# Optimization experiments

Hardware: AMD Instinct MI355X
Metric: run time of the kernel (lower is better)

The kernel has to match this reference:

```python
import jax, jax.numpy as jnp
import numpy as np

DIM = 512
D_STATE = 16
D_CONV = 4
EXPAND = 2
D_INNER = EXPAND * DIM  # 1024
BATCH = 4
SEQLEN = 4096


def silu(v):
    return v * jax.nn.sigmoid(v)


def setup_inputs() -> dict:
    key = jax.random.key(0)
    ks = jax.random.split(key, 8)
    s = 0.02  # small init scale for stability
    return {
        "x": jax.random.normal(ks[0], (BATCH, SEQLEN, DIM), jnp.float32),
        "W_in": jax.random.normal(ks[1], (2 * D_INNER, DIM), jnp.float32) * s,
        "conv_w": jax.random.normal(ks[2], (D_INNER, 1, D_CONV), jnp.float32) * s,
        "conv_b": jax.random.normal(ks[3], (D_INNER,), jnp.float32) * s,
        "W_x": jax.random.normal(ks[4], (2 * D_STATE, D_INNER), jnp.float32) * s,
        "W_dt": jax.random.normal(ks[5], (D_STATE, D_INNER), jnp.float32) * s,
        "b_dt": jax.random.normal(ks[6], (D_STATE,), jnp.float32) * s,
        "A_log": jnp.log(jnp.arange(1, D_STATE + 1, dtype=jnp.float32))[None, :],
        "D_param": jnp.ones((D_INNER,), jnp.float32),
        "W_out": jax.random.normal(ks[7], (DIM, D_INNER), jnp.float32) * s,
    }


def reference(x, W_in, conv_w, conv_b, W_x, W_dt, b_dt, A_log, D_param, W_out):
    B, L, _ = x.shape
    # in_proj and split into x / res streams
    x_and_res = jnp.einsum('bld,ed->ble', x, W_in)          # [B,L,2*d_inner]
    xi, res = x_and_res[..., :D_INNER], x_and_res[..., D_INNER:]
    # causal depthwise conv1d (torch pads both sides by d_conv-1 then slices [:L]
    # == left-pad d_conv-1, no right pad)
    xc = jax.lax.conv_general_dilated(
        xi.transpose(0, 2, 1), conv_w, (1,), [(D_CONV - 1, 0)],
        dimension_numbers=('NCH', 'OIH', 'NCH'), feature_group_count=D_INNER)
    xa = silu(xc.transpose(0, 2, 1) + conv_b)               # [B,L,d_inner]
    # x_proj: first d_state (dt) half is discarded in the source; keep B half
    B_proj = jnp.einsum('bld,ed->ble', xa, W_x)[..., D_STATE:]  # [B,L,N]
    dt = jax.nn.softplus(jnp.einsum('bld,nd->bln', xa, W_dt) + b_dt)  # [B,L,N]
    A = -jnp.exp(A_log.reshape(-1))                         # [N]
    A_disc = jnp.exp(A * dt)                                # [B,L,N]
    d_rep = D_INNER // D_STATE
    u = jnp.mean(xa[..., :d_rep], axis=-1)                  # [B,L] scalar drive
    Bu = (dt * B_proj) * u[..., None]                       # [B,L,N]

    def step(s, ab):
        a, b = ab
        s = s * a + b
        return s, s

    s0 = jnp.zeros((B, D_STATE), xa.dtype)
    _, y = jax.lax.scan(step, s0, (A_disc.transpose(1, 0, 2), Bu.transpose(1, 0, 2)))
    y = y.transpose(1, 0, 2)                                # [B,L,N]
    y = jnp.repeat(y, d_rep, axis=-1)                       # [B,L,d_inner]
    y = y + xa * D_param
    y = y * silu(res)
    return jnp.einsum('bld,ed->ble', y, W_out)              # [B,L,dim]
```

## Files before the change

kernel.cpp:

```cpp
#include <hip/hip_runtime.h>
#include <stdint.h>

typedef __bf16 bf16_t;
typedef __bf16 bf16x8 __attribute__((ext_vector_type(8)));
typedef __bf16 bf16x4 __attribute__((ext_vector_type(4)));
typedef float  f32x4  __attribute__((ext_vector_type(4)));

#define AS1 __attribute__((address_space(1)))
#define AS3 __attribute__((address_space(3)))

#define SEQ   4096
#define DIMM  512
#define DIN   1024
#define ROWS  16384

__device__ __forceinline__ void gload_lds16(const void* g, void* l) {
  __builtin_amdgcn_global_load_lds((AS1 void*)g, (AS3 void*)l, 16, 0, 0);
}

template<bool OUT_BF16>
__global__ void gemm_bt(const bf16_t* __restrict__ A, const bf16_t* __restrict__ B,
                        void* __restrict__ Cv, int lda, int N, int K)
{
  __shared__ __align__(16) bf16_t As[128*64];
  __shared__ __align__(16) bf16_t Bs[128*64];
  const int tid = threadIdx.x;
  const int l = tid & 63, w = tid >> 6;
  const int bm = blockIdx.x, bn = blockIdx.y;
  const bf16_t* Ab = A + (size_t)bm*128*lda;
  const bf16_t* Bb = B + (size_t)bn*128*K;
  f32x4 acc[4][4] = {};
  const int wr = (w>>1)*64, wc = (w&1)*64;
  const int lr = l & 15, lk = (l>>4)*8;
  const int srow = w*8 + (l>>3);
  const int scol = (l&7)*8;

  for (int kt = 0; kt < K; kt += 64) {
#pragma unroll
    for (int i = 0; i < 4; i++) {
      gload_lds16(Ab + (size_t)(i*32 + srow)*lda + kt + scol, As + i*2048 + w*512);
      gload_lds16(Bb + (size_t)(i*32 + srow)*K   + kt + scol, Bs + i*2048 + w*512);
    }
    __syncthreads();
#pragma unroll
    for (int kk = 0; kk < 2; kk++) {
      bf16x8 af[4], bv[4];
#pragma unroll
      for (int m = 0; m < 4; m++) af[m] = *(const bf16x8*)&As[(wr + m*16 + lr)*64 + kk*32 + lk];
#pragma unroll
      for (int n = 0; n < 4; n++) bv[n] = *(const bf16x8*)&Bs[(wc + n*16 + lr)*64 + kk*32 + lk];
#pragma unroll
      for (int m = 0; m < 4; m++)
#pragma unroll
        for (int n = 0; n < 4; n++)
          acc[m][n] = __builtin_amdgcn_mfma_f32_16x16x32_bf16(af[m], bv[n], acc[m][n], 0, 0, 0);
    }
    __syncthreads();
  }
  const int row0 = bm*128 + wr + (l>>4)*4;
  const int col0 = bn*128 + wc + lr;
#pragma unroll
  for (int m = 0; m < 4; m++)
#pragma unroll
    for (int n = 0; n < 4; n++)
#pragma unroll
      for (int r = 0; r < 4; r++) {
        size_t idx = (size_t)(row0 + m*16 + r)*N + (col0 + n*16);
        if constexpr (OUT_BF16) ((bf16_t*)Cv)[idx] = (bf16_t)acc[m][n][r];
        else                    ((float*)Cv)[idx]  = acc[m][n][r];
      }
}

__global__ __launch_bounds__(256) void convert_kernel(
    const float* __restrict__ x, const float* __restrict__ W_in,
    const float* __restrict__ W_out, const float* __restrict__ W_dt, const float* __restrict__ W_x,
    bf16_t* __restrict__ x_bf, bf16_t* __restrict__ Win_bf,
    bf16_t* __restrict__ Wout_bf, bf16_t* __restrict__ Wcat_bf)
{
  const size_t N0 = 8388608/4, N1 = N0 + 1048576/4, N2 = N1 + 524288/4, N3 = N2 + 131072/4;
  size_t i = (size_t)blockIdx.x*256 + threadIdx.x;
  bf16_t* dst; float4 v;
  if (i < N0)      { v = ((const float4*)x)[i];          dst = x_bf   + i*4; }
  else if (i < N1) { size_t j = i - N0; v = ((const float4*)W_in)[j];  dst = Win_bf  + j*4; }
  else if (i < N2) { size_t j = i - N1; v = ((const float4*)W_out)[j]; dst = Wout_bf + j*4; }
  else if (i < N3) {
    size_t j = i - N2; size_t el = j*4; int r = (int)(el >> 10), c = (int)(el & 1023);
    if (r < 16)      v = *(const float4*)(W_dt + r*1024 + c);
    else if (r < 32) v = *(const float4*)(W_x  + r*1024 + c);
    else             v = make_float4(0.f, 0.f, 0.f, 0.f);
    dst = Wcat_bf + el;
  } else return;
  bf16x4 o; o[0]=(bf16_t)v.x; o[1]=(bf16_t)v.y; o[2]=(bf16_t)v.z; o[3]=(bf16_t)v.w;
  *(bf16x4*)dst = o;
}

#define CONV_T 16
__global__ __launch_bounds__(256) void conv_kernel(
    const bf16_t* __restrict__ xi_res, const float* __restrict__ conv_w,
    const float* __restrict__ conv_b, bf16_t* __restrict__ xa, float* __restrict__ u)
{
  const int team = blockIdx.x*2 + (threadIdx.x >> 7);
  const int t    = threadIdx.x & 127;
  const int b    = team >> 8;
  const int r0   = (team & 255) * CONV_T;
  const int c0   = t * 8;

  float w[8][4], bias[8];
#pragma unroll
  for (int e = 0; e < 8; e++) {
    float4 v = *(const float4*)(conv_w + (size_t)(c0 + e)*4);
    w[e][0]=v.x; w[e][1]=v.y; w[e][2]=v.z; w[e][3]=v.w;
  }
  {
    float4 b0 = *(const float4*)(conv_b + c0);
    float4 b1 = *(const float4*)(conv_b + c0 + 4);
    bias[0]=b0.x; bias[1]=b0.y; bias[2]=b0.z; bias[3]=b0.w;
    bias[4]=b1.x; bias[5]=b1.y; bias[6]=b1.z; bias[7]=b1.w;
  }

  const bf16_t* xbase = xi_res + (size_t)b*SEQ*2048 + c0;
  bf16x8 win[4];
#pragma unroll
  for (int k = 0; k < 4; k++)
#pragma unroll
    for (int e = 0; e < 8; e++) win[k][e] = (bf16_t)0.f;

#pragma unroll
  for (int k = 1; k < 4; k++) {
    int lb = r0 - 4 + k;
    if (lb >= 0) win[k] = *(const bf16x8*)(xbase + (size_t)lb*2048);
  }

  const int growbase = b*SEQ + r0;
#pragma unroll
  for (int i = 0; i < CONV_T; i++) {
    win[i & 3] = *(const bf16x8*)(xbase + (size_t)(r0 + i)*2048);
    bf16x8 o;
    float usum = 0.f;
#pragma unroll
    for (int e = 0; e < 8; e++) {
      float acc = bias[e]
        + w[e][0]*(float)win[(i+1)&3][e]
        + w[e][1]*(float)win[(i+2)&3][e]
        + w[e][2]*(float)win[(i+3)&3][e]
        + w[e][3]*(float)win[(i  )&3][e];
      float sil = acc / (1.f + expf(-acc));
      usum += sil;
      o[e] = (bf16_t)sil;
    }
    *(bf16x8*)(xa + (size_t)(growbase + i)*DIN + c0) = o;
    if (t < 8) {
      usum += __shfl_xor(usum, 1, 64);
      usum += __shfl_xor(usum, 2, 64);
      usum += __shfl_xor(usum, 4, 64);
      if (t == 0) u[growbase + i] = usum * (1.f/64.f);
    }
  }
}

__global__ __launch_bounds__(256) void dt_kernel(
    const float* __restrict__ proj, const float* __restrict__ u,
    const float* __restrict__ b_dt, const float* __restrict__ A_log, float2* __restrict__ aBu)
{
  int idx = blockIdx.x*256 + threadIdx.x;
  int row = idx >> 4, n = idx & 15;
  float xdt = proj[(size_t)row*128 + n] + b_dt[n];
  float dt = (xdt > 20.f) ? xdt : log1pf(expf(xdt));
  float a  = expf(-expf(A_log[n]) * dt);
  float Bu = dt * proj[(size_t)row*128 + 16 + n] * u[row];
  aBu[idx] = make_float2(a, Bu);
}

__global__ __launch_bounds__(64) void scan_kernel(const float2* __restrict__ aBu, float* __restrict__ y)
{
  const int b = blockIdx.x >> 4, n = blockIdx.x & 15;
  const int l = threadIdx.x;
  const float2* base = aBu + (size_t)b*SEQ*16 + n;
  const int t0 = l*64;
  float P = 1.f, S = 0.f;
  for (int s = 0; s < 64; s++) {
    float2 ab = base[(size_t)(t0+s)*16];
    S = S*ab.x + ab.y;
    P *= ab.x;
  }
  float Pi = P, Si = S;
#pragma unroll
  for (int off = 1; off < 64; off <<= 1) {
    float Pp = __shfl_up(Pi, off, 64);
    float Sp = __shfl_up(Si, off, 64);
    if (l >= off) { Si = Sp*Pi + Si; Pi *= Pp; }
  }
  float carry = __shfl_up(Si, 1, 64);
  if (l == 0) carry = 0.f;
  float s = carry;
  float* yb = y + (size_t)b*SEQ*16 + n;
  for (int st = 0; st < 64; st++) {
    float2 ab = base[(size_t)(t0+st)*16];
    s = s*ab.x + ab.y;
    yb[(size_t)(t0+st)*16] = s;
  }
}

__global__ __launch_bounds__(256) void yfull_kernel(
    const bf16_t* __restrict__ xa, bf16_t* __restrict__ xi_res,
    const float* __restrict__ y_state, const float* __restrict__ D_param)
{
  int idx = blockIdx.x*256 + threadIdx.x;
  int row = idx >> 7, cc = (idx & 127)*8;
  bf16x8 xav  = *(const bf16x8*)&xa[(size_t)row*DIN + cc];
  bf16x8 resv = *(const bf16x8*)&xi_res[(size_t)row*2048 + DIN + cc];
  float ys = y_state[(size_t)row*16 + (cc >> 6)];
  float dp[8];
  float4 d0 = *(const float4*)(D_param + cc);
  float4 d1 = *(const float4*)(D_param + cc + 4);
  dp[0]=d0.x; dp[1]=d0.y; dp[2]=d0.z; dp[3]=d0.w; dp[4]=d1.x; dp[5]=d1.y; dp[6]=d1.z; dp[7]=d1.w;
  bf16x8 o;
#pragma unroll
  for (int e = 0; e < 8; e++) {
    float r = (float)resv[e];
    float sil = r / (1.f + expf(-r));
    float yv = (ys + (float)xav[e]*dp[e]) * sil;
    o[e] = (bf16_t)yv;
  }
  *(bf16x8*)&xi_res[(size_t)row*2048 + cc] = o;
}

extern "C" void kernel_launch(void* const* d_in, const int* in_sizes, int n_in,
                              void* d_out, int out_size, void* d_ws, size_t ws_size,
                              hipStream_t stream)
{
  const float* x      = (const float*)d_in[0];
  const float* W_in   = (const float*)d_in[1];
  const float* conv_w = (const float*)d_in[2];
  const float* conv_b = (const float*)d_in[3];
  const float* W_x    = (const float*)d_in[4];
  const float* W_dt   = (const float*)d_in[5];
  const float* b_dt   = (const float*)d_in[6];
  const float* A_log  = (const float*)d_in[7];
  const float* D_param= (const float*)d_in[8];
  const float* W_out  = (const float*)d_in[9];
  float* out = (float*)d_out;
  char* ws = (char*)d_ws;

  if (ws_size < 121700352u) return;

  const size_t MB = 1024*1024;
  bf16_t* x_bf    = (bf16_t*)(ws + 0);
  float*  proj    = (float*) (ws + 0);
  float*  y_state = (float*) (ws + 8*MB);
  bf16_t* Win_bf  = (bf16_t*)(ws + 16*MB);
  float2* aBu     = (float2*)(ws + 16*MB);
  bf16_t* Wout_bf = (bf16_t*)(ws + 18*MB);
  bf16_t* Wcat_bf = (bf16_t*)(ws + 19*MB);
  bf16_t* xi_res  = (bf16_t*)(ws + 20*MB);
  bf16_t* xa      = (bf16_t*)(ws + 84*MB);
  float*  u       = (float*) (ws + 116*MB);

  convert_kernel<<<dim3(9856), dim3(256), 0, stream>>>(x, W_in, W_out, W_dt, W_x,
                                                       x_bf, Win_bf, Wout_bf, Wcat_bf);
  gemm_bt<true ><<<dim3(128,16), dim3(256), 0, stream>>>(x_bf, Win_bf, (void*)xi_res, 512, 2048, 512);
  conv_kernel   <<<dim3(512), dim3(256), 0, stream>>>(xi_res, conv_w, conv_b, xa, u);
  gemm_bt<false><<<dim3(128,1), dim3(256), 0, stream>>>(xa, Wcat_bf, (void*)proj, 1024, 128, 1024);
  dt_kernel     <<<dim3(1024), dim3(256), 0, stream>>>(proj, u, b_dt, A_log, aBu);
  scan_kernel   <<<dim3(64), dim3(64), 0, stream>>>(aBu, y_state);
  yfull_kernel  <<<dim3(8192), dim3(256), 0, stream>>>(xa, xi_res, y_state, D_param);
  gemm_bt<false><<<dim3(128,4), dim3(256), 0, stream>>>(xi_res, Wout_bf, (void*)out, 2048, 512, 1024);
}
```

Before: 249.7 us.

## Fuse dt/softplus into projection GEMM epilogue and rework scan layout

The dt/softplus/A_disc/Bu computation moves into the epilogue of the x_proj GEMM, which writes aBu directly in a [batch, state, seq] layout, so the separate dt kernel and the proj round trip go away. The scan kernel now uses 256 threads per (batch, state) sequence, staging the contiguous sequence in LDS with padding and doing a two-level warp plus block scan, instead of strided global loads by 64 threads. yfull reads y_state in the new transposed layout. This trades strided yfull reads and heavier GEMM epilogue work for fewer launches and a shorter serial scan.

Result: no change. 245.8 us (-1.6%).

```diff
diff --git a/kernel.cpp b/kernel.cpp
--- a/kernel.cpp
+++ b/kernel.cpp
@@ -18,9 +18,11 @@
   __builtin_amdgcn_global_load_lds((AS1 void*)g, (AS3 void*)l, 16, 0, 0);
 }
 
-template<bool OUT_BF16>
+template<int MODE>
 __global__ void gemm_bt(const bf16_t* __restrict__ A, const bf16_t* __restrict__ B,
-                        void* __restrict__ Cv, int lda, int N, int K)
+                        void* __restrict__ Cv, int lda, int N, int K,
+                        const float* __restrict__ u_g, const float* __restrict__ b_dt_g,
+                        const float* __restrict__ A_log_g)
 {
   __shared__ __align__(16) bf16_t As[128*64];
   __shared__ __align__(16) bf16_t Bs[128*64];
@@ -59,6 +61,28 @@
   }
   const int row0 = bm*128 + wr + (l>>4)*4;
   const int col0 = bn*128 + wc + lr;
+
+  if constexpr (MODE == 2) {
+    if (wc == 0) {
+      const float bdt  = b_dt_g[lr];
+      const float Aexp = expf(A_log_g[lr]);
+      float2* aBu = (float2*)Cv;
+#pragma unroll
+      for (int m = 0; m < 4; m++)
+#pragma unroll
+        for (int r = 0; r < 4; r++) {
+          int row = row0 + m*16 + r;
+          float xdt = acc[m][0][r] + bdt;
+          float dt  = (xdt > 20.f) ? xdt : log1pf(expf(xdt));
+          float a   = expf(-Aexp * dt);
+          float Bu  = dt * acc[m][1][r] * u_g[row];
+          int b = row >> 12, li = row & 4095;
+          aBu[(size_t)((b<<4) + lr)*4096 + li] = make_float2(a, Bu);
+        }
+    }
+    return;
+  }
+
 #pragma unroll
   for (int m = 0; m < 4; m++)
 #pragma unroll
@@ -66,8 +90,8 @@
 #pragma unroll
       for (int r = 0; r < 4; r++) {
         size_t idx = (size_t)(row0 + m*16 + r)*N + (col0 + n*16);
-        if constexpr (OUT_BF16) ((bf16_t*)Cv)[idx] = (bf16_t)acc[m][n][r];
-        else                    ((float*)Cv)[idx]  = acc[m][n][r];
+        if constexpr (MODE == 1) ((bf16_t*)Cv)[idx] = (bf16_t)acc[m][n][r];
+        else                     ((float*)Cv)[idx]  = acc[m][n][r];
       }
 }
 
@@ -158,46 +182,64 @@
   }
 }
 
-__global__ __launch_bounds__(256) void dt_kernel(
-    const float* __restrict__ proj, const float* __restrict__ u,
-    const float* __restrict__ b_dt, const float* __restrict__ A_log, float2* __restrict__ aBu)
-{
-  int idx = blockIdx.x*256 + threadIdx.x;
-  int row = idx >> 4, n = idx & 15;
-  float xdt = proj[(size_t)row*128 + n] + b_dt[n];
-  float dt = (xdt > 20.f) ? xdt : log1pf(expf(xdt));
-  float a  = expf(-expf(A_log[n]) * dt);
-  float Bu = dt * proj[(size_t)row*128 + 16 + n] * u[row];
-  aBu[idx] = make_float2(a, Bu);
-}
-
-__global__ __launch_bounds__(64) void scan_kernel(const float2* __restrict__ aBu, float* __restrict__ y)
-{
-  const int b = blockIdx.x >> 4, n = blockIdx.x & 15;
-  const int l = threadIdx.x;
-  const float2* base = aBu + (size_t)b*SEQ*16 + n;
-  const int t0 = l*64;
+__global__ __launch_bounds__(256) void scan_kernel(const float2* __restrict__ aBu, float* __restrict__ y)
+{
+  __shared__ float2 lds[4096 + 256];
+  __shared__ float2 wtot[4];
+  const int tid = threadIdx.x;
+  const int bn = blockIdx.x;
+  const float2* base = aBu + (size_t)bn*4096;
+
+#pragma unroll
+  for (int c = 0; c < 16; c++) {
+    int i = c*256 + tid;
+    lds[i + (i>>4)] = base[i];
+  }
+  __syncthreads();
+
+  const int p0 = tid*17;
   float P = 1.f, S = 0.f;
-  for (int s = 0; s < 64; s++) {
-    float2 ab = base[(size_t)(t0+s)*16];
+#pragma unroll
+  for (int j = 0; j < 16; j++) {
+    float2 ab = lds[p0 + j];
     S = S*ab.x + ab.y;
     P *= ab.x;
   }
   float Pi = P, Si = S;
+  const int l = tid & 63;
 #pragma unroll
   for (int off = 1; off < 64; off <<= 1) {
     float Pp = __shfl_up(Pi, off, 64);
     float Sp = __shfl_up(Si, off, 64);
-    if (l >= off) { Si = Sp*Pi + Si; Pi *= Pp; }
-  }
-  float carry = __shfl_up(Si, 1, 64);
-  if (l == 0) carry = 0.f;
-  float s = carry;
-  float* yb = y + (size_t)b*SEQ*16 + n;
-  for (int st = 0; st < 64; st++) {
-    float2 ab = base[(size_t)(t0+st)*16];
+    if (l >= off) { Si = Sp*Pi + Si; Pi = Pp*Pi; }
+  }
+  const int w = tid >> 6;
+  if (l == 63) wtot[w] = make_float2(Pi, Si);
+  __syncthreads();
+
+  float Pc = 1.f, Sc = 0.f;
+  for (int k = 0; k < 4; k++)
+    if (k < w) { Sc = Sc*wtot[k].x + wtot[k].y; Pc *= wtot[k].x; }
+  float Pe = 1.f, Se = 0.f;
+  {
+    float Pp = __shfl_up(Pi, 1, 64);
+    float Sp = __shfl_up(Si, 1, 64);
+    if (l > 0) { Pe = Pp; Se = Sp; }
+  }
+  float s = Sc*Pe + Se;
+
+#pragma unroll
+  for (int j = 0; j < 16; j++) {
+    float2 ab = lds[p0 + j];
     s = s*ab.x + ab.y;
-    yb[(size_t)(t0+st)*16] = s;
+    lds[p0 + j].x = s;
+  }
+  __syncthreads();
+  float* yb = y + (size_t)bn*4096;
+#pragma unroll
+  for (int c = 0; c < 16; c++) {
+    int i = c*256 + tid;
+    yb[i] = lds[i + (i>>4)].x;
   }
 }
 
@@ -209,7 +251,8 @@
   int row = idx >> 7, cc = (idx & 127)*8;
   bf16x8 xav  = *(const bf16x8*)&xa[(size_t)row*DIN + cc];
   bf16x8 resv = *(const bf16x8*)&xi_res[(size_t)row*2048 + DIN + cc];
-  float ys = y_state[(size_t)row*16 + (cc >> 6)];
+  int b = row >> 12, li = row & 4095, n = cc >> 6;
+  float ys = y_state[(size_t)((b<<4) + n)*4096 + li];
   float dp[8];
   float4 d0 = *(const float4*)(D_param + cc);
   float4 d1 = *(const float4*)(D_param + cc + 4);
@@ -246,7 +289,6 @@
 
   const size_t MB = 1024*1024;
   bf16_t* x_bf    = (bf16_t*)(ws + 0);
-  float*  proj    = (float*) (ws + 0);
   float*  y_state = (float*) (ws + 8*MB);
   bf16_t* Win_bf  = (bf16_t*)(ws + 16*MB);
   float2* aBu     = (float2*)(ws + 16*MB);
@@ -258,11 +300,13 @@
 
   convert_kernel<<<dim3(9856), dim3(256), 0, stream>>>(x, W_in, W_out, W_dt, W_x,
                                                        x_bf, Win_bf, Wout_bf, Wcat_bf);
-  gemm_bt<true ><<<dim3(128,16), dim3(256), 0, stream>>>(x_bf, Win_bf, (void*)xi_res, 512, 2048, 512);
-  conv_kernel   <<<dim3(512), dim3(256), 0, stream>>>(xi_res, conv_w, conv_b, xa, u);
-  gemm_bt<false><<<dim3(128,1), dim3(256), 0, stream>>>(xa, Wcat_bf, (void*)proj, 1024, 128, 1024);
-  dt_kernel     <<<dim3(1024), dim3(256), 0, stream>>>(proj, u, b_dt, A_log, aBu);
-  scan_kernel   <<<dim3(64), dim3(64), 0, stream>>>(aBu, y_state);
-  yfull_kernel  <<<dim3(8192), dim3(256), 0, stream>>>(xa, xi_res, y_state, D_param);
-  gemm_bt<false><<<dim3(128,4), dim3(256), 0, stream>>>(xi_res, Wout_bf, (void*)out, 2048, 512, 1024);
-}
+  gemm_bt<1><<<dim3(128,16), dim3(256), 0, stream>>>(x_bf, Win_bf, (void*)xi_res, 512, 2048, 512,
+                                                     nullptr, nullptr, nullptr);
+  conv_kernel<<<dim3(512), dim3(256), 0, stream>>>(xi_res, conv_w, conv_b, xa, u);
+  gemm_bt<2><<<dim3(128,1), dim3(256), 0, stream>>>(xa, Wcat_bf, (void*)aBu, 1024, 128, 1024,
+                                                    u, b_dt, A_log);
+  scan_kernel<<<dim3(64), dim3(256), 0, stream>>>(aBu, y_state);
+  yfull_kernel<<<dim3(8192), dim3(256), 0, stream>>>(xa, xi_res, y_state, D_param);
+  gemm_bt<0><<<dim3(128,4), dim3(256), 0, stream>>>(xi_res, Wout_bf, (void*)out, 2048, 512, 1024,
+                                                    nullptr, nullptr, nullptr);
+}
```
